# Optimization experiments

Measured on AMD Instinct MI355X. Metric: run time of the kernel, lower is better.

Reference implementation:

```python
import jax, jax.numpy as jnp
import numpy as np

B, N, D_IN, D_EMB = 8, 2048, 768, 768

def setup_inputs() -> dict:
    key = jax.random.key(0)
    k1, k2, k3, k4 = jax.random.split(key, 4)
    x = jax.random.normal(k1, (B, N, D_IN), dtype=jnp.float32)
    # nn.Linear weights stored as [out, in]; applied as x @ W.T
    Wq = jax.random.normal(k2, (D_EMB, D_IN), dtype=jnp.float32) * (D_IN ** -0.5)
    Wk = jax.random.normal(k3, (D_EMB, D_IN), dtype=jnp.float32) * (D_IN ** -0.5)
    Wv = jax.random.normal(k4, (D_EMB, D_IN), dtype=jnp.float32) * (D_IN ** -0.5)
    return {"x": x, "Wq": Wq, "Wk": Wk, "Wv": Wv}

def reference(x, Wq, Wk, Wv):
    dim_sqrt = jnp.asarray(D_EMB ** 0.5, x.dtype)
    q = jnp.einsum('bnd,ed->bne', x, Wq)  # [B,N,E]
    k = jnp.einsum('bnd,ed->bne', x, Wk)
    v = jnp.einsum('bnd,ed->bne', x, Wv)
    scores = jnp.einsum('bne,bme->bnm', q, k)  # [B,N,N]
    # NOTE: module applies softmax FIRST, then divides by sqrt(d) (post-hoc)
    attn = jax.nn.softmax(scores, axis=-1) / dim_sqrt
    out = jnp.einsum('bnm,bme->bne', attn, v)
    return out
```

## Files before the change

### kernel.cpp

```cpp
#include <hip/hip_runtime.h>
#include <stdint.h>
#include <type_traits>

typedef __bf16 bf16;
typedef _Float16 f16;
typedef bf16 bf16x8 __attribute__((ext_vector_type(8)));
typedef f16 f16x8 __attribute__((ext_vector_type(8)));
typedef float f32x4 __attribute__((ext_vector_type(4)));

#define LOG2E 1.4426950408889634f
#define SQRT_E 27.712812921102035f

enum { EPI_F32 = 0, EPI_PAIR = 1, EPI_VT = 2, EPI_F16 = 3 };

__device__ __forceinline__ void async16(const void* g, void* l) {
  __builtin_amdgcn_global_load_lds(
      (__attribute__((address_space(1))) void*)(uintptr_t)g,
      (__attribute__((address_space(3))) void*)l, 16, 0, 0);
}

__device__ __forceinline__ f32x4 mfma8(bf16x8 a, bf16x8 b, f32x4 c) {
  return __builtin_amdgcn_mfma_f32_16x16x32_bf16(a, b, c, 0, 0, 0);
}
__device__ __forceinline__ f32x4 mfma8(f16x8 a, f16x8 b, f32x4 c) {
  return __builtin_amdgcn_mfma_f32_16x16x32_f16(a, b, c, 0, 0, 0);
}

template <int N>
__device__ __forceinline__ void vwait() {
  asm volatile("s_waitcnt vmcnt(%0)" ::"i"(N) : "memory");
}
__device__ __forceinline__ void block_bar() {
  asm volatile("" ::: "memory");
  __builtin_amdgcn_s_barrier();
  asm volatile("" ::: "memory");
}
__device__ __forceinline__ void lgkm0() {
  asm volatile("s_waitcnt lgkmcnt(0)" ::: "memory");
}
__device__ __forceinline__ void spin() { __builtin_amdgcn_sched_barrier(0); }

__global__ __launch_bounds__(512, 2)
void s_ring(const f16* __restrict__ Ah, const f16* __restrict__ Bh,
            f16* __restrict__ Pt, float* __restrict__ mxg,
            float* __restrict__ smg) {
  __shared__ __align__(16) char smem[98304];
  f16* sAb = (f16*)smem;
  f16* sBb = (f16*)(smem + 49152);

  const int id = blockIdx.x;
  const int xcd = id & 7;
  const int j0 = id >> 3;
  const int s = j0 >> 3;
  const int bxi = j0 & 7;
  const int g = xcd + 8 * s;
  const int z = g & 7;
  const int byi = g >> 3;

  const f16* pA = Ah + (long)z * 1572864;
  const f16* pB = Bh + (long)z * 1572864;

  const int bm = byi * 256;
  const int bn = bxi * 256;
  const int tid = threadIdx.x;
  const int wave = tid >> 6;
  const int lane = tid & 63;
  const int wm = (wave >> 2) * 128;
  const int wn = (wave & 3) * 64;
  const int quad = lane >> 4;
  const int l16 = lane & 15;

  f32x4 acc[8][4] = {};

  const int srow = tid >> 2;
  const int swc = ((tid & 3) ^ ((tid >> 3) & 3)) * 8;
  const int cread = (quad ^ ((l16 >> 1) & 3)) * 8;

  constexpr int NT = 24;
  constexpr int LPT = 4;

  auto stageA = [&](int buf, int t, int l) {
    const long ka = (long)t * 32 + swc;
    async16(pA + (long)(bm + l * 128 + srow) * 768 + ka,
            &sAb[buf * 8192 + (l * 512 + tid) * 8]);
  };
  auto stageB = [&](int buf, int t, int l) {
    const long ka = (long)t * 32 + swc;
    async16(pB + (long)(bn + l * 128 + srow) * 768 + ka,
            &sBb[buf * 8192 + (l * 512 + tid) * 8]);
  };

  stageA(0, 0, 0); stageA(0, 0, 1); stageB(0, 0, 0); stageB(0, 0, 1);
  stageA(1, 1, 0); stageA(1, 1, 1); stageB(1, 1, 0); stageB(1, 1, 1);
  vwait<LPT>();
  block_bar();

  auto tile_step = [&](int t, int cur, int b2) {
    const bool st = (t + 2 < NT);
    f16x8 bfr[4], af[4];
#pragma unroll
    for (int j = 0; j < 4; ++j)
      bfr[j] = *(const f16x8*)&sBb[cur * 8192 + (wn + j * 16 + l16) * 32 + cread];
#pragma unroll
    for (int i = 0; i < 4; ++i)
      af[i] = *(const f16x8*)&sAb[cur * 8192 + (wm + i * 16 + l16) * 32 + cread];
    if (st) { stageA(b2, t + 2, 0); stageA(b2, t + 2, 1); }
    block_bar();
    lgkm0();
    spin();
    __builtin_amdgcn_s_setprio(1);
#pragma unroll
    for (int j = 0; j < 4; ++j)
#pragma unroll
      for (int i = 0; i < 4; ++i)
        acc[i][j] = mfma8(af[i], bfr[j], acc[i][j]);
    __builtin_amdgcn_s_setprio(0);
    spin();
    block_bar();
    f16x8 af2[4];
#pragma unroll
    for (int i = 0; i < 4; ++i)
      af2[i] = *(const f16x8*)&sAb[cur * 8192 + (wm + 64 + i * 16 + l16) * 32 + cread];
    if (st) { stageB(b2, t + 2, 0); stageB(b2, t + 2, 1); }
    block_bar();
    lgkm0();
    spin();
    __builtin_amdgcn_s_setprio(1);
#pragma unroll
    for (int j = 0; j < 4; ++j)
#pragma unroll
      for (int i = 0; i < 4; ++i)
        acc[4 + i][j] = mfma8(af2[i], bfr[j], acc[4 + i][j]);
    __builtin_amdgcn_s_setprio(0);
    spin();
    if (t + 1 < NT) {
      if (st) vwait<LPT>(); else vwait<0>();
      block_bar();
    }
  };

  for (int p = 0; p < NT / 3; ++p) {
    const int t = p * 3;
    tile_step(t + 0, 0, 2);
    tile_step(t + 1, 1, 0);
    tile_step(t + 2, 2, 1);
  }

  block_bar();
  float* red = (float*)smem;
  const int wnid = wave & 3;
  float m_[8][4];
  {
    float mx_[8][4];
#pragma unroll
    for (int i = 0; i < 8; ++i)
#pragma unroll
      for (int r = 0; r < 4; ++r) {
        float v = fmaxf(fmaxf(acc[i][0][r], acc[i][1][r]),
                        fmaxf(acc[i][2][r], acc[i][3][r]));
#pragma unroll
        for (int o = 8; o >= 1; o >>= 1) v = fmaxf(v, __shfl_xor(v, o));
        mx_[i][r] = v;
      }
    if (l16 == 0) {
#pragma unroll
      for (int i = 0; i < 8; ++i)
#pragma unroll
        for (int r = 0; r < 4; ++r)
          red[(wm + i * 16 + quad * 4 + r) * 4 + wnid] = mx_[i][r];
    }
  }
  block_bar();
#pragma unroll
  for (int i = 0; i < 8; ++i)
#pragma unroll
    for (int r = 0; r < 4; ++r) {
      const f32x4 v = *(const f32x4*)&red[(wm + i * 16 + quad * 4 + r) * 4];
      m_[i][r] = fmaxf(fmaxf(v[0], v[1]), fmaxf(v[2], v[3]));
    }
  {
    float sm_[8][4];
#pragma unroll
    for (int i = 0; i < 8; ++i)
#pragma unroll
      for (int r = 0; r < 4; ++r) {
        float ssum = 0.f;
#pragma unroll
        for (int j = 0; j < 4; ++j) {
          const float e = exp2f((acc[i][j][r] - m_[i][r]) * LOG2E);
          acc[i][j][r] = e;
          ssum += e;
        }
#pragma unroll
        for (int o = 8; o >= 1; o >>= 1) ssum += __shfl_xor(ssum, o);
        sm_[i][r] = ssum;
      }
    if (l16 == 0) {
#pragma unroll
      for (int i = 0; i < 8; ++i)
#pragma unroll
        for (int r = 0; r < 4; ++r)
          red[1024 + (wm + i * 16 + quad * 4 + r) * 4 + wnid] = sm_[i][r];
    }
  }
  block_bar();
  if (wnid == 0 && l16 == 0) {
    float* mxo = mxg + ((long)z * 8 + bxi) * 2048 + bm;
    float* smo = smg + ((long)z * 8 + bxi) * 2048 + bm;
#pragma unroll
    for (int i = 0; i < 8; ++i)
#pragma unroll
      for (int r = 0; r < 4; ++r) {
        const int row = wm + i * 16 + quad * 4 + r;
        const f32x4 v = *(const f32x4*)&red[1024 + row * 4];
        mxo[row] = m_[i][r];
        smo[row] = (v[0] + v[1]) + (v[2] + v[3]);
      }
  }

  lgkm0();
  f16* P = Pt + (long)z * 4194304;
  f16* pk = (f16*)smem;
  constexpr int PP = 264;
  const int hi = wave >> 2;
#pragma unroll
  for (int half = 0; half < 2; ++half) {
    block_bar();
    if (hi == half) {
#pragma unroll
      for (int i = 0; i < 8; ++i)
#pragma unroll
        for (int r = 0; r < 4; ++r) {
          const int row = i * 16 + quad * 4 + r;
#pragma unroll
          for (int j = 0; j < 4; ++j)
            pk[row * PP + wn + j * 16 + l16] = (f16)acc[i][j][r];
        }
    }
    block_bar();
#pragma unroll
    for (int k = 0; k < 8; ++k) {
      const int c = k * 512 + tid;
      const int row = c >> 5;
      const int ch = c & 31;
      const uint4 v = *(const uint4*)&pk[row * PP + ch * 8];
      *(uint4*)&P[(long)(bm + half * 128 + row) * 2048 + bn + ch * 8] = v;
    }
  }
}

__global__ __launch_bounds__(256)
void combine(const float* __restrict__ mxg, const float* __restrict__ smg,
             float* __restrict__ gam) {
  const int R = blockIdx.x * 256 + threadIdx.x;
  const int z = R >> 11, m = R & 2047;
  float mx[8], sm[8];
#pragma unroll
  for (int t = 0; t < 8; ++t) {
    mx[t] = mxg[((long)z * 8 + t) * 2048 + m];
    sm[t] = smg[((long)z * 8 + t) * 2048 + m];
  }
  float M = mx[0];
#pragma unroll
  for (int t = 1; t < 8; ++t) M = fmaxf(M, mx[t]);
  float S = 0.f;
#pragma unroll
  for (int t = 0; t < 8; ++t) S += sm[t] * exp2f((mx[t] - M) * LOG2E);
  const float inv = 1.0f / (S * SQRT_E);
#pragma unroll
  for (int t = 0; t < 8; ++t)
    gam[(long)t * 16384 + R] = exp2f((mx[t] - M) * LOG2E) * inv;
}

__global__ __launch_bounds__(256, 2)
void pv_pipe(const f16* __restrict__ Pt, const f16* __restrict__ Vt,
             const float* __restrict__ gam, float* __restrict__ out) {
  constexpr int LPT = 8;
  __shared__ __align__(16) f16 sA[2][128 * 64];
  __shared__ __align__(16) f16 sB[2][128 * 64];

  const int id = blockIdx.x;
  const int xcd = id & 7;
  const int j0 = id >> 3;
  const int s = j0 / 6;
  const int bxi = j0 - s * 6;
  const int g = xcd + 8 * s;
  const int byi = g & 15;
  const int z = g >> 4;

  const f16* pA = Pt + (long)z * 4194304;
  const f16* pB = Vt + (long)z * 1572864;

  const int bm = byi * 128;
  const int bn = bxi * 128;
  const int tid = threadIdx.x;
  const int wave = tid >> 6;
  const int lane = tid & 63;
  const int wm = (wave >> 1) * 64;
  const int wn = (wave & 1) * 64;
  const int quad = lane >> 4;
  const int l16 = lane & 15;

  f32x4 accM[4][4] = {};
  f32x4 accT[4][4] = {};

  const int srow = tid >> 3;
  const int schk = tid & 7;
  const int swc = (schk ^ (srow & 7)) * 8;
  const int cs0 = (quad * 8) ^ ((l16 & 7) << 3);

  auto stage = [&](int buf, int t) {
    const long ka = (long)t * 64 + swc;
#pragma unroll
    for (int l = 0; l < 4; ++l)
      async16(pA + (long)(bm + l * 32 + srow) * 2048 + ka,
              &sA[buf][(l * 256 + tid) * 8]);
#pragma unroll
    for (int l = 0; l < 4; ++l)
      async16(pB + (long)(bn + l * 32 + srow) * 2048 + ka,
              &sB[buf][(l * 256 + tid) * 8]);
  };

  auto compute = [&](int buf) {
    f16x8 bf[2][4];
#pragma unroll
    for (int kk = 0; kk < 2; ++kk)
#pragma unroll
      for (int jj = 0; jj < 4; ++jj)
        bf[kk][jj] = *(const f16x8*)&sB[buf][(wn + jj * 16 + l16) * 64 +
                                            (cs0 ^ (kk * 32))];
#pragma unroll
    for (int mq = 0; mq < 2; ++mq) {
      f16x8 af[2][2];
#pragma unroll
      for (int kk = 0; kk < 2; ++kk)
#pragma unroll
        for (int ii = 0; ii < 2; ++ii)
          af[kk][ii] =
              *(const f16x8*)&sA[buf][(wm + mq * 32 + ii * 16 + l16) * 64 +
                                      (cs0 ^ (kk * 32))];
      __builtin_amdgcn_s_setprio(1);
#pragma unroll
      for (int jj = 0; jj < 4; ++jj)
#pragma unroll
        for (int ii = 0; ii < 2; ++ii)
#pragma unroll
          for (int kk = 0; kk < 2; ++kk)
            accT[mq * 2 + ii][jj] =
                mfma8(af[kk][ii], bf[kk][jj], accT[mq * 2 + ii][jj]);
      __builtin_amdgcn_s_setprio(0);
    }
  };

  stage(0, 0);
  stage(1, 1);
  vwait<LPT>();
  block_bar();

  f32x4 gv[4];
  constexpr int NT = 32;
  for (int t = 0; t < NT; ++t) {
    const int cur = t & 1;
    if ((t & 3) == 0) {
      const float* gp = gam + ((long)(t >> 2) * 16384 + z * 2048 + bm + wm);
#pragma unroll
      for (int i = 0; i < 4; ++i)
        gv[i] = *(const f32x4*)&gp[i * 16 + quad * 4];
    }
    compute(cur);
    if ((t & 3) == 3) {
#pragma unroll
      for (int i = 0; i < 4; ++i)
#pragma unroll
        for (int j = 0; j < 4; ++j)
#pragma unroll
          for (int r = 0; r < 4; ++r) {
            accM[i][j][r] += gv[i][r] * accT[i][j][r];
            accT[i][j][r] = 0.f;
          }
    }
    if (t + 1 < NT) {
      block_bar();
      if (t + 2 < NT) { stage(cur, t + 2); vwait<LPT>(); }
      else vwait<0>();
      block_bar();
    }
  }

  float* C = out + (long)z * 1572864;
#pragma unroll
  for (int i = 0; i < 4; ++i) {
    const int mb = bm + wm + i * 16 + quad * 4;
#pragma unroll
    for (int j = 0; j < 4; ++j) {
      const int n = bn + wn + j * 16 + l16;
#pragma unroll
      for (int r = 0; r < 4; ++r)
        C[(long)(mb + r) * 768 + n] = accM[i][j][r];
    }
  }
}

template <typename T, typename TO, int BMt, int BNt, int BKt, int AT, int EPI>
__global__ __launch_bounds__((BMt == 256 ? 512 : 256), 2)
void gemm_pipe(const T* __restrict__ Ah, const T* __restrict__ Al,
               const T* __restrict__ Bh, void* __restrict__ C0,
               int K, long lda, long ldb, long ldc,
               long stA, long stB, long stC, int gxN, int gyM) {
  using vec8 = typename std::conditional<std::is_same<T, bf16>::value,
                                         bf16x8, f16x8>::type;
  static_assert(BMt == BNt, "square tiles only");
  constexpr int THREADS = (BMt == 256) ? 512 : 256;
  constexpr int NWN = (BMt == 256) ? 4 : 2;
  constexpr int WTM = BMt / 2;
  constexpr int WTN = BNt / NWN;
  static_assert(WTN == 64, "wave tile must be 64 wide");
  constexpr int MF = WTM / 16;
  constexpr int KK = BKt / 32;
  constexpr int CPR = BKt / 8;
  constexpr int RPI = THREADS / CPR;
  constexpr int LPP = (BMt * BKt) / (THREADS * 8);
  constexpr int LPT = LPP * (AT == 2 ? 3 : 2);

  __shared__ __align__(16) T sA[2][BMt * BKt];
  __shared__ __align__(16) T sB[2][BNt * BKt];
  __shared__ __align__(16) T sAl[AT == 2 ? 2 * BMt * BKt : 8];

  const int id = blockIdx.x;
  const int xcd = id & 7;
  const int j0 = id >> 3;
  const int s = j0 / gxN;
  const int bxi = j0 - s * gxN;
  const int g = xcd + 8 * s;
  const int byi = g % gyM;
  const int z = g / gyM;

  const T* pA = Ah + (long)z * stA;
  const T* pB = Bh + (long)z * stB;
  const T* pAl = (AT == 2) ? Al : nullptr;

  const int bm = byi * BMt;
  const int bn = bxi * BNt;
  const int tid = threadIdx.x;
  const int wave = tid >> 6;
  const int lane = tid & 63;
  const int wm = (wave / NWN) * WTM;
  const int wn = (wave % NWN) * WTN;
  const int quad = lane >> 4;
  const int l16 = lane & 15;

  f32x4 acc[MF][4] = {};

  const int srow = tid / CPR;
  const int schk = tid % CPR;
  const int swc = ((BKt == 64) ? (schk ^ (srow & 7)) : schk) * 8;
  const int cs0 = (quad * 8) ^ ((BKt == 64) ? ((l16 & 7) << 3) : 0);

  const int NT = K / BKt;

  auto stage = [&](int buf, int t) {
    const long ka = (long)t * BKt + swc;
#pragma unroll
    for (int l = 0; l < LPP; ++l)
      async16(pA + (long)(bm + l * RPI + srow) * lda + ka,
              &sA[buf][(l * THREADS + tid) * 8]);
#pragma unroll
    for (int l = 0; l < LPP; ++l)
      async16(pB + (long)(bn + l * RPI + srow) * ldb + ka,
              &sB[buf][(l * THREADS + tid) * 8]);
    if constexpr (AT == 2) {
#pragma unroll
      for (int l = 0; l < LPP; ++l)
        async16(pAl + (long)(bm + l * RPI + srow) * lda + ka,
                &sAl[buf * BMt * BKt + (l * THREADS + tid) * 8]);
    }
  };

  auto compute = [&](int buf) {
    const T* bA = &sA[buf][0];
    const T* bB = &sB[buf][0];
    const T* bAl = (AT == 2) ? &sAl[buf * BMt * BKt] : nullptr;
    vec8 bf[KK][4];
#pragma unroll
    for (int kk = 0; kk < KK; ++kk)
#pragma unroll
      for (int jj = 0; jj < 4; ++jj)
        bf[kk][jj] =
            *(const vec8*)&bB[(wn + jj * 16 + l16) * BKt + (cs0 ^ (kk * 32))];
#pragma unroll
    for (int mq = 0; mq < MF / 2; ++mq) {
      vec8 af[KK][2];
      vec8 alf[AT == 2 ? KK : 1][2];
#pragma unroll
      for (int kk = 0; kk < KK; ++kk)
#pragma unroll
        for (int ii = 0; ii < 2; ++ii) {
          const int r = wm + mq * 32 + ii * 16 + l16;
          af[kk][ii] = *(const vec8*)&bA[r * BKt + (cs0 ^ (kk * 32))];
          if constexpr (AT == 2)
            alf[kk][ii] = *(const vec8*)&bAl[r * BKt + (cs0 ^ (kk * 32))];
        }
      __builtin_amdgcn_s_setprio(1);
#pragma unroll
      for (int jj = 0; jj < 4; ++jj)
#pragma unroll
        for (int ii = 0; ii < 2; ++ii)
#pragma unroll
          for (int kk = 0; kk < KK; ++kk) {
            acc[mq * 2 + ii][jj] =
                mfma8(af[kk][ii], bf[kk][jj], acc[mq * 2 + ii][jj]);
            if constexpr (AT == 2)
              acc[mq * 2 + ii][jj] =
                  mfma8(alf[kk][ii], bf[kk][jj], acc[mq * 2 + ii][jj]);
          }
      __builtin_amdgcn_s_setprio(0);
    }
  };

  stage(0, 0);
  stage(1, 1);
  vwait<LPT>();
  block_bar();

  for (int t = 0; t < NT; ++t) {
    const int cur = t & 1;
    compute(cur);
    if (t + 1 < NT) {
      block_bar();
      if (t + 2 < NT) {
        stage(cur, t + 2);
        vwait<LPT>();
      } else {
        vwait<0>();
      }
      block_bar();
    }
  }

  if constexpr (EPI == EPI_F16) {
    TO* Ch = (TO*)C0;
#pragma unroll
    for (int i = 0; i < MF; ++i) {
      const int mb = bm + wm + i * 16 + quad * 4;
#pragma unroll
      for (int j = 0; j < 4; ++j) {
        const int n = bn + wn + j * 16 + l16;
#pragma unroll
        for (int r = 0; r < 4; ++r)
          Ch[(long)(mb + r) * ldc + n] = (TO)acc[i][j][r];
      }
    }
  } else if constexpr (EPI == EPI_VT) {
    TO* vT = (TO*)C0;
#pragma unroll
    for (int i = 0; i < MF; ++i) {
      const int mb = bm + wm + i * 16 + quad * 4;
      const long bb = mb >> 11;
      const long ml = mb & 2047;
#pragma unroll
      for (int j = 0; j < 4; ++j) {
        const int e = bn + wn + j * 16 + l16;
        union { TO b[4]; uint2 u; } P;
#pragma unroll
        for (int r = 0; r < 4; ++r) P.b[r] = (TO)acc[i][j][r];
        *(uint2*)&vT[(bb * 768 + e) * 2048 + ml] = P.u;
      }
    }
  } else {
    float* C = (float*)C0 + (long)z * stC;
#pragma unroll
    for (int i = 0; i < MF; ++i) {
      const int mb = bm + wm + i * 16 + quad * 4;
#pragma unroll
      for (int j = 0; j < 4; ++j) {
        const int n = bn + wn + j * 16 + l16;
#pragma unroll
        for (int r = 0; r < 4; ++r)
          C[(long)(mb + r) * ldc + n] = acc[i][j][r];
      }
    }
  }
}

constexpr int BM = 128, BN = 128, BK = 64;

template <typename T, typename TO, int AT, int BT, int EPI, int SWZ>
__global__ __launch_bounds__(256)
void gemm_kernel(const T* __restrict__ Ah, const T* __restrict__ Al,
                 const T* __restrict__ Bh, const T* __restrict__ Bl,
                 void* __restrict__ C0, void* __restrict__ C1,
                 int K, long lda, long ldb, long ldbl, long ldc,
                 long stA, long stB, long stBl, long stC,
                 int gxN, int gyM) {
  using vec8 = typename std::conditional<std::is_same<T, bf16>::value,
                                         bf16x8, f16x8>::type;
  __shared__ __align__(16) T sAh[BM * BK];
  __shared__ __align__(16) T sBh[BN * BK];
  __shared__ __align__(16) T sAl[AT == 2 ? BM * BK : 8];
  __shared__ __align__(16) T sBl[BT == 2 ? BN * BK : 8];

  int bxi, byi, z;
  if constexpr (SWZ) {
    const int id = blockIdx.x;
    const int xcd = id & 7;
    const int j = id >> 3;
    const int s = j / gxN;
    const int n = j - s * gxN;
    const int g = xcd + 8 * s;
    bxi = n;
    byi = g % gyM;
    z = g / gyM;
  } else {
    bxi = blockIdx.x; byi = blockIdx.y; z = blockIdx.z;
  }

  const T* pAh = Ah + (long)z * stA;
  const T* pBh = Bh + (long)z * stB;
  const T* pAl = (AT == 2) ? (Al + (long)z * stA) : nullptr;
  const T* pBl = (BT == 2) ? (Bl + (long)z * stBl) : nullptr;

  const int bm = byi * BM;
  const int bn = bxi * BN;
  const int tid = threadIdx.x;
  const int wave = tid >> 6;
  const int lane = tid & 63;
  const int wm = (wave & 1) * 64;
  const int wn = (wave >> 1) * 64;
  const int quad = lane >> 4;
  const int l16 = lane & 15;

  f32x4 acc[4][4] = {};

  const int sr0 = tid >> 3;
  const int swc = ((tid & 7) ^ (sr0 & 7)) * 8;
  const int cs0 = (quad * 8) ^ ((l16 & 7) << 3);

  for (int kt = 0; kt < K; kt += BK) {
    __syncthreads();
    {
      const long ka = kt + swc;
#pragma unroll
      for (int l = 0; l < 4; ++l) {
        const int row = l * 32 + sr0;
        async16(pAh + (long)(bm + row) * lda + ka, &sAh[(l * 256 + tid) * 8]);
      }
#pragma unroll
      for (int l = 0; l < 4; ++l) {
        const int row = l * 32 + sr0;
        async16(pBh + (long)(bn + row) * ldb + ka, &sBh[(l * 256 + tid) * 8]);
      }
      if constexpr (AT == 2) {
#pragma unroll
        for (int l = 0; l < 4; ++l) {
          const int row = l * 32 + sr0;
          async16(pAl + (long)(bm + row) * lda + ka, &sAl[(l * 256 + tid) * 8]);
        }
      }
      if constexpr (BT == 2) {
#pragma unroll
        for (int l = 0; l < 4; ++l) {
          const int row = l * 32 + sr0;
          async16(pBl + (long)(bn + row) * ldbl + ka, &sBl[(l * 256 + tid) * 8]);
        }
      }
    }
    __syncthreads();

#pragma unroll
    for (int kk = 0; kk < 2; ++kk) {
      const int cs = cs0 ^ (kk * 32);
      vec8 ah[4], al[4];
#pragma unroll
      for (int i = 0; i < 4; ++i) {
        ah[i] = *(const vec8*)&sAh[(wm + i * 16 + l16) * BK + cs];
        if constexpr (AT == 2)
          al[i] = *(const vec8*)&sAl[(wm + i * 16 + l16) * BK + cs];
      }
#pragma unroll
      for (int j = 0; j < 4; ++j) {
        const vec8 bh = *(const vec8*)&sBh[(wn + j * 16 + l16) * BK + cs];
        vec8 bl;
        if constexpr (BT == 2)
          bl = *(const vec8*)&sBl[(wn + j * 16 + l16) * BK + cs];
#pragma unroll
        for (int i = 0; i < 4; ++i) {
          acc[i][j] = mfma8(ah[i], bh, acc[i][j]);
          if constexpr (BT == 2) acc[i][j] = mfma8(ah[i], bl, acc[i][j]);
          if constexpr (AT == 2) acc[i][j] = mfma8(al[i], bh, acc[i][j]);
        }
      }
    }
  }

  if constexpr (EPI == EPI_PAIR) {
    TO* Ch = (TO*)C0;
    TO* Cl = (TO*)C1;
#pragma unroll
    for (int i = 0; i < 4; ++i) {
      const int mb = bm + wm + i * 16 + quad * 4;
#pragma unroll
      for (int j = 0; j < 4; ++j) {
        const int n = bn + wn + j * 16 + l16;
#pragma unroll
        for (int r = 0; r < 4; ++r) {
          const float f = acc[i][j][r];
          const TO h = (TO)f;
          const long idx = (long)(mb + r) * ldc + n;
          Ch[idx] = h;
          Cl[idx] = (TO)(f - (float)h);
        }
      }
    }
  }
}

__global__ __launch_bounds__(256)
void split_all(const float4* __restrict__ x, const float4* __restrict__ wv,
               uint2* __restrict__ xh, uint2* __restrict__ xl,
               uint2* __restrict__ wvh) {
  constexpr int NX = 3145728;
  constexpr int NWV = 147456;
  const int i = blockIdx.x * 256 + threadIdx.x;
  float4 v;
  uint2 *dh, *dl;
  if (i < NX) {
    v = x[i]; dh = xh + i; dl = xl + i;
  } else {
    const int m = i - NX;
    if (m >= NWV) return;
    v = wv[m]; dh = wvh + m; dl = nullptr;
  }
  const f16 h0 = (f16)v.x, h1 = (f16)v.y, h2 = (f16)v.z, h3 = (f16)v.w;
  union { f16 b[4]; uint2 u; } P;
  P.b[0] = h0; P.b[1] = h1; P.b[2] = h2; P.b[3] = h3;
  *dh = P.u;
  if (dl != nullptr) {
    P.b[0] = (f16)(v.x - (float)h0);
    P.b[1] = (f16)(v.y - (float)h1);
    P.b[2] = (f16)(v.z - (float)h2);
    P.b[3] = (f16)(v.w - (float)h3);
    *dl = P.u;
  }
}

__global__ __launch_bounds__(256)
void transpose_split(const float* __restrict__ Wq, const float* __restrict__ Wk,
                     f16* __restrict__ qTh, f16* __restrict__ qTl,
                     f16* __restrict__ kTh, f16* __restrict__ kTl) {
  __shared__ float tile[64][65];
  const float* src = blockIdx.z ? Wk : Wq;
  f16* dh = blockIdx.z ? kTh : qTh;
  f16* dl = blockIdx.z ? kTl : qTl;
  const int e0 = blockIdx.y * 64, d0 = blockIdx.x * 64;
  const int t = threadIdx.x;
  const int r = t >> 2;
  const int c4 = (t & 3) * 16;
  const float4* s4 = (const float4*)(src + (long)(e0 + r) * 768 + d0 + c4);
#pragma unroll
  for (int g = 0; g < 4; ++g) {
    const float4 v = s4[g];
    tile[r][c4 + g * 4 + 0] = v.x;
    tile[r][c4 + g * 4 + 1] = v.y;
    tile[r][c4 + g * 4 + 2] = v.z;
    tile[r][c4 + g * 4 + 3] = v.w;
  }
  __syncthreads();
  union { f16 b[8]; uint4 u; } H0, H1, L0, L1;
#pragma unroll
  for (int i = 0; i < 16; ++i) {
    const float v = tile[c4 + i][r];
    const f16 h = (f16)v;
    const f16 l = (f16)(v - (float)h);
    if (i < 8) { H0.b[i] = h; L0.b[i] = l; }
    else       { H1.b[i - 8] = h; L1.b[i - 8] = l; }
  }
  const long o = (long)(d0 + r) * 768 + e0 + c4;
  *(uint4*)(dh + o) = H0.u;  *(uint4*)(dh + o + 8) = H1.u;
  *(uint4*)(dl + o) = L0.u;  *(uint4*)(dl + o + 8) = L1.u;
}

extern "C" void kernel_launch(void* const* d_in, const int* in_sizes, int n_in,
                              void* d_out, int out_size, void* d_ws, size_t ws_size,
                              hipStream_t stream) {
  const float* x  = (const float*)d_in[0];
  const float* Wq = (const float*)d_in[1];
  const float* Wk = (const float*)d_in[2];
  const float* Wv = (const float*)d_in[3];
  float* out = (float*)d_out;
  char* ws = (char*)d_ws;

  const size_t SZ = 25165824;
  f16* yh = (f16*)(ws + 0 * SZ);
  f16* xh = (f16*)(ws + 2 * SZ);
  f16* vT = (f16*)(ws + 3 * SZ);
  const size_t PERS = 4 * SZ;
  const size_t WT = 1179648;
  f16* xl   = (f16*)(ws + PERS);
  f16* wqTh = (f16*)(ws + PERS + SZ);
  f16* wqTl = (f16*)(ws + PERS + SZ + 1 * WT);
  f16* wkTh = (f16*)(ws + PERS + SZ + 2 * WT);
  f16* wkTl = (f16*)(ws + PERS + SZ + 3 * WT);
  f16* mtH  = (f16*)(ws + PERS + SZ + 4 * WT);
  f16* mtL  = (f16*)(ws + PERS + SZ + 5 * WT);
  f16* wvh  = (f16*)(ws + PERS + SZ + 6 * WT);
  f16* Pt = (f16*)(ws + PERS);
  float* mxg = (float*)(ws + PERS + 67108864);
  float* smg = mxg + 131072;
  float* gam = smg + 131072;

  split_all<<<12864, 256, 0, stream>>>(
      (const float4*)x, (const float4*)Wv, (uint2*)xh, (uint2*)xl, (uint2*)wvh);
  transpose_split<<<dim3(12, 12, 2), 256, 0, stream>>>(
      Wq, Wk, wqTh, wqTl, wkTh, wkTl);

  gemm_kernel<f16, f16, 2, 2, EPI_PAIR, 0><<<dim3(6, 6, 1), 256, 0, stream>>>(
      wkTh, wkTl, wqTh, wqTl, (void*)mtH, (void*)mtL,
      768, 768, 768, 768, 768, 0, 0, 0, 0, 0, 0);

  gemm_pipe<f16, f16, 128, 128, 32, 2, EPI_F16><<<768, 256, 0, stream>>>(
      xh, xl, mtH, (void*)yh, 768, 768, 768, 768, 0, 0, 0, 6, 128);

  gemm_pipe<f16, f16, 128, 128, 64, 1, EPI_VT><<<768, 256, 0, stream>>>(
      xh, nullptr, wvh, (void*)vT, 768, 768, 768, 0, 0, 0, 0, 6, 128);

  s_ring<<<512, 512, 0, stream>>>(yh, xh, Pt, mxg, smg);
  combine<<<64, 256, 0, stream>>>(mxg, smg, gam);
  pv_pipe<<<768, 256, 0, stream>>>(Pt, vT, gam, out);
}
```

Baseline: 402.2 us.

## Store raw fp32 scores and apply softmax normalization inside PV kernel

Measured after the change: 424.6 us. 5.6% more time.

```diff
diff --git a/kernel.cpp b/kernel.cpp
--- a/kernel.cpp
+++ b/kernel.cpp
@@ -42,7 +42,7 @@
 
 __global__ __launch_bounds__(512, 2)
 void s_ring(const f16* __restrict__ Ah, const f16* __restrict__ Bh,
-            f16* __restrict__ Pt, float* __restrict__ mxg,
+            float* __restrict__ Sc, float* __restrict__ mxg,
             float* __restrict__ smg) {
   __shared__ __align__(16) char smem[98304];
   f16* sAb = (f16*)smem;
@@ -146,6 +146,19 @@
     tile_step(t + 2, 2, 1);
   }
 
+  float* C = Sc + (long)z * 4194304;
+#pragma unroll
+  for (int i = 0; i < 8; ++i) {
+    const int mb = bm + wm + i * 16 + quad * 4;
+#pragma unroll
+    for (int j = 0; j < 4; ++j) {
+      const int n = bn + wn + j * 16 + l16;
+#pragma unroll
+      for (int r = 0; r < 4; ++r)
+        C[(long)(mb + r) * 2048 + n] = acc[i][j][r];
+    }
+  }
+
   block_bar();
   float* red = (float*)smem;
   const int wnid = wave & 3;
@@ -170,6 +183,7 @@
           red[(wm + i * 16 + quad * 4 + r) * 4 + wnid] = mx_[i][r];
     }
   }
+  lgkm0();
   block_bar();
 #pragma unroll
   for (int i = 0; i < 8; ++i)
@@ -186,15 +200,14 @@
       for (int r = 0; r < 4; ++r) {
         float ssum = 0.f;
 #pragma unroll
-        for (int j = 0; j < 4; ++j) {
-          const float e = exp2f((acc[i][j][r] - m_[i][r]) * LOG2E);
-          acc[i][j][r] = e;
-          ssum += e;
-        }
+        for (int j = 0; j < 4; ++j)
+          ssum += exp2f((acc[i][j][r] - m_[i][r]) * LOG2E);
 #pragma unroll
         for (int o = 8; o >= 1; o >>= 1) ssum += __shfl_xor(ssum, o);
         sm_[i][r] = ssum;
       }
+    lgkm0();
+    block_bar();
     if (l16 == 0) {
 #pragma unroll
       for (int i = 0; i < 8; ++i)
@@ -203,6 +216,7 @@
           red[1024 + (wm + i * 16 + quad * 4 + r) * 4 + wnid] = sm_[i][r];
     }
   }
+  lgkm0();
   block_bar();
   if (wnid == 0 && l16 == 0) {
     float* mxo = mxg + ((long)z * 8 + bxi) * 2048 + bm;
@@ -217,41 +231,11 @@
         smo[row] = (v[0] + v[1]) + (v[2] + v[3]);
       }
   }
-
-  lgkm0();
-  f16* P = Pt + (long)z * 4194304;
-  f16* pk = (f16*)smem;
-  constexpr int PP = 264;
-  const int hi = wave >> 2;
-#pragma unroll
-  for (int half = 0; half < 2; ++half) {
-    block_bar();
-    if (hi == half) {
-#pragma unroll
-      for (int i = 0; i < 8; ++i)
-#pragma unroll
-        for (int r = 0; r < 4; ++r) {
-          const int row = i * 16 + quad * 4 + r;
-#pragma unroll
-          for (int j = 0; j < 4; ++j)
-            pk[row * PP + wn + j * 16 + l16] = (f16)acc[i][j][r];
-        }
-    }
-    block_bar();
-#pragma unroll
-    for (int k = 0; k < 8; ++k) {
-      const int c = k * 512 + tid;
-      const int row = c >> 5;
-      const int ch = c & 31;
-      const uint4 v = *(const uint4*)&pk[row * PP + ch * 8];
-      *(uint4*)&P[(long)(bm + half * 128 + row) * 2048 + bn + ch * 8] = v;
-    }
-  }
 }
 
 __global__ __launch_bounds__(256)
 void combine(const float* __restrict__ mxg, const float* __restrict__ smg,
-             float* __restrict__ gam) {
+             float* __restrict__ nrm) {
   const int R = blockIdx.x * 256 + threadIdx.x;
   const int z = R >> 11, m = R & 2047;
   float mx[8], sm[8];
@@ -266,16 +250,15 @@
   float S = 0.f;
 #pragma unroll
   for (int t = 0; t < 8; ++t) S += sm[t] * exp2f((mx[t] - M) * LOG2E);
-  const float inv = 1.0f / (S * SQRT_E);
-#pragma unroll
-  for (int t = 0; t < 8; ++t)
-    gam[(long)t * 16384 + R] = exp2f((mx[t] - M) * LOG2E) * inv;
+  float2 o;
+  o.x = -M * LOG2E;
+  o.y = 1.0f / (S * SQRT_E);
+  *(float2*)&nrm[(long)R * 2] = o;
 }
 
 __global__ __launch_bounds__(256, 2)
-void pv_pipe(const f16* __restrict__ Pt, const f16* __restrict__ Vt,
-             const float* __restrict__ gam, float* __restrict__ out) {
-  constexpr int LPT = 8;
+void pv_norm(const float* __restrict__ Sc, const f16* __restrict__ Vt,
+             const float* __restrict__ nrm, float* __restrict__ out) {
   __shared__ __align__(16) f16 sA[2][128 * 64];
   __shared__ __align__(16) f16 sB[2][128 * 64];
 
@@ -288,7 +271,7 @@
   const int byi = g & 15;
   const int z = g >> 4;
 
-  const f16* pA = Pt + (long)z * 4194304;
+  const float* pA = Sc + (long)z * 4194304;
   const f16* pB = Vt + (long)z * 1572864;
 
   const int bm = byi * 128;
@@ -301,24 +284,51 @@
   const int quad = lane >> 4;
   const int l16 = lane & 15;
 
-  f32x4 accM[4][4] = {};
-  f32x4 accT[4][4] = {};
+  f32x4 acc[4][4] = {};
 
   const int srow = tid >> 3;
   const int schk = tid & 7;
   const int swc = (schk ^ (srow & 7)) * 8;
   const int cs0 = (quad * 8) ^ ((l16 & 7) << 3);
 
-  auto stage = [&](int buf, int t) {
+  float nmx[4], ninv[4];
+#pragma unroll
+  for (int l = 0; l < 4; ++l) {
+    const int r = bm + l * 32 + srow;
+    const float2 mv = *(const float2*)&nrm[((long)z * 2048 + r) * 2];
+    nmx[l] = mv.x; ninv[l] = mv.y;
+  }
+
+  float4 ra[4][2];
+  auto issueA = [&](int t) {
+    const long co = (long)t * 64 + swc;
+#pragma unroll
+    for (int l = 0; l < 4; ++l) {
+      const float* p = pA + (long)(bm + l * 32 + srow) * 2048 + co;
+      ra[l][0] = *(const float4*)p;
+      ra[l][1] = *(const float4*)(p + 4);
+    }
+  };
+  auto stageB = [&](int buf, int t) {
     const long ka = (long)t * 64 + swc;
-#pragma unroll
-    for (int l = 0; l < 4; ++l)
-      async16(pA + (long)(bm + l * 32 + srow) * 2048 + ka,
-              &sA[buf][(l * 256 + tid) * 8]);
 #pragma unroll
     for (int l = 0; l < 4; ++l)
       async16(pB + (long)(bn + l * 32 + srow) * 2048 + ka,
               &sB[buf][(l * 256 + tid) * 8]);
+  };
+  auto writeA = [&](int buf) {
+#pragma unroll
+    for (int l = 0; l < 4; ++l) {
+      union { f16 h[8]; uint4 u; } P;
+      const float* a0 = (const float*)&ra[l][0];
+      const float* a1 = (const float*)&ra[l][1];
+#pragma unroll
+      for (int e = 0; e < 4; ++e) {
+        P.h[e]     = (f16)(exp2f(fmaf(a0[e], LOG2E, nmx[l])) * ninv[l]);
+        P.h[e + 4] = (f16)(exp2f(fmaf(a1[e], LOG2E, nmx[l])) * ninv[l]);
+      }
+      *(uint4*)&sA[buf][(l * 256 + tid) * 8] = P.u;
+    }
   };
 
   auto compute = [&](int buf) {
@@ -346,44 +356,31 @@
         for (int ii = 0; ii < 2; ++ii)
 #pragma unroll
           for (int kk = 0; kk < 2; ++kk)
-            accT[mq * 2 + ii][jj] =
-                mfma8(af[kk][ii], bf[kk][jj], accT[mq * 2 + ii][jj]);
+            acc[mq * 2 + ii][jj] =
+                mfma8(af[kk][ii], bf[kk][jj], acc[mq * 2 + ii][jj]);
       __builtin_amdgcn_s_setprio(0);
     }
   };
 
-  stage(0, 0);
-  stage(1, 1);
-  vwait<LPT>();
+  issueA(0);
+  stageB(0, 0);
+  vwait<0>();
+  writeA(0);
+  lgkm0();
   block_bar();
 
-  f32x4 gv[4];
   constexpr int NT = 32;
+  int cur = 0;
   for (int t = 0; t < NT; ++t) {
-    const int cur = t & 1;
-    if ((t & 3) == 0) {
-      const float* gp = gam + ((long)(t >> 2) * 16384 + z * 2048 + bm + wm);
-#pragma unroll
-      for (int i = 0; i < 4; ++i)
-        gv[i] = *(const f32x4*)&gp[i * 16 + quad * 4];
-    }
+    if (t + 1 < NT) { issueA(t + 1); stageB(cur ^ 1, t + 1); }
+    spin();
     compute(cur);
-    if ((t & 3) == 3) {
-#pragma unroll
-      for (int i = 0; i < 4; ++i)
-#pragma unroll
-        for (int j = 0; j < 4; ++j)
-#pragma unroll
-          for (int r = 0; r < 4; ++r) {
-            accM[i][j][r] += gv[i][r] * accT[i][j][r];
-            accT[i][j][r] = 0.f;
-          }
-    }
     if (t + 1 < NT) {
+      vwait<0>();
+      writeA(cur ^ 1);
+      lgkm0();
       block_bar();
-      if (t + 2 < NT) { stage(cur, t + 2); vwait<LPT>(); }
-      else vwait<0>();
-      block_bar();
+      cur ^= 1;
     }
   }
 
@@ -396,7 +393,7 @@
       const int n = bn + wn + j * 16 + l16;
 #pragma unroll
       for (int r = 0; r < 4; ++r)
-        C[(long)(mb + r) * 768 + n] = accM[i][j][r];
+        C[(long)(mb + r) * 768 + n] = acc[i][j][r];
     }
   }
 }
@@ -791,6 +788,9 @@
 
   const size_t SZ = 25165824;
   f16* yh = (f16*)(ws + 0 * SZ);
+  float* mxg = (float*)(ws + SZ);
+  float* smg = (float*)(ws + SZ + 2097152);
+  float* nrm = (float*)(ws + SZ + 4194304);
   f16* xh = (f16*)(ws + 2 * SZ);
   f16* vT = (f16*)(ws + 3 * SZ);
   const size_t PERS = 4 * SZ;
@@ -803,10 +803,7 @@
   f16* mtH  = (f16*)(ws + PERS + SZ + 4 * WT);
   f16* mtL  = (f16*)(ws + PERS + SZ + 5 * WT);
   f16* wvh  = (f16*)(ws + PERS + SZ + 6 * WT);
-  f16* Pt = (f16*)(ws + PERS);
-  float* mxg = (float*)(ws + PERS + 67108864);
-  float* smg = mxg + 131072;
-  float* gam = smg + 131072;
+  float* scores = (float*)(ws + PERS);
 
   split_all<<<12864, 256, 0, stream>>>(
       (const float4*)x, (const float4*)Wv, (uint2*)xh, (uint2*)xl, (uint2*)wvh);
@@ -823,7 +820,7 @@
   gemm_pipe<f16, f16, 128, 128, 64, 1, EPI_VT><<<768, 256, 0, stream>>>(
       xh, nullptr, wvh, (void*)vT, 768, 768, 768, 0, 0, 0, 0, 6, 128);
 
-  s_ring<<<512, 512, 0, stream>>>(yh, xh, Pt, mxg, smg);
-  combine<<<64, 256, 0, stream>>>(mxg, smg, gam);
-  pv_pipe<<<768, 256, 0, stream>>>(Pt, vT, gam, out);
-}
+  s_ring<<<512, 512, 0, stream>>>(yh, xh, scores, mxg, smg);
+  combine<<<64, 256, 0, stream>>>(mxg, smg, nrm);
+  pv_norm<<<768, 256, 0, stream>>>(scores, vT, nrm, out);
+}
```
